# Performance work log

Measured on AMD Instinct MI355X. Metric: run time of the kernel, lower is better.

## Reference

```python
import jax, jax.numpy as jnp
import numpy as np

PAD = 0.1
RESO = 128           # plane_resolution
HID = 128            # hidden_dim
CDIM = 128           # c_dim
NBLK = 5             # n_blocks
PLANES = (('xz', (0, 2)), ('xy', (0, 1)), ('yz', (1, 2)))


def normalize_coordinate(p, dims):
    # p: (B,T,3) -> (B,T,2) in [0, 1)
    xy = p[..., list(dims)] / (1.0 + PAD + 1e-3) + 0.5
    return jnp.clip(xy, 0.0, 1.0 - 1e-5)


def coordinate2index(xy, reso):
    g = (xy * reso).astype(jnp.int32)          # (B,T,2)
    return g[..., 0] + reso * g[..., 1]        # (B,T) flat cell index


def scatter_max_gather(vals, idx, n_cells):
    # vals: (B,T,F), idx: (B,T) -> per-cell max gathered back to points (B,T,F)
    B, T, F = vals.shape
    flat_idx = (idx + jnp.arange(B, dtype=idx.dtype)[:, None] * n_cells).reshape(-1)
    fea = jax.ops.segment_max(vals.reshape(B * T, F), flat_idx, num_segments=B * n_cells)
    return fea[flat_idx].reshape(B, T, F)


def scatter_mean_plane(c, idx, n_cells):
    # c: (B,T,C), idx: (B,T) -> (B, n_cells, C); empty cells stay 0
    B, T, C = c.shape
    flat_idx = (idx + jnp.arange(B, dtype=idx.dtype)[:, None] * n_cells).reshape(-1)
    s = jax.ops.segment_sum(c.reshape(B * T, C), flat_idx, num_segments=B * n_cells)
    cnt = jax.ops.segment_sum(jnp.ones((B * T,), c.dtype), flat_idx, num_segments=B * n_cells)
    return (s / jnp.maximum(cnt, 1.0)[:, None]).reshape(B, n_cells, C)


def resnet_block(x, W0, b0, W1, b1, Ws):
    # ResnetBlockFC(2H -> H), size_h = H, shortcut = Linear(no bias)
    net = jax.nn.relu(x) @ W0 + b0
    dx = jax.nn.relu(net) @ W1 + b1
    return x @ Ws + dx


def setup_inputs() -> dict:
    key = jax.random.key(0)
    ks = jax.random.split(key, 10)
    B, T = 2, 32768
    s = 0.05
    return {
        'p': jax.random.uniform(ks[0], (B, T, 3), jnp.float32, -0.5, 0.5),
        'fc_pos_W': s * jax.random.normal(ks[1], (3, 2 * HID), jnp.float32),
        'fc_pos_b': s * jax.random.normal(ks[2], (2 * HID,), jnp.float32),
        'blocks_W0': s * jax.random.normal(ks[3], (NBLK, 2 * HID, HID), jnp.float32),
        'blocks_b0': s * jax.random.normal(ks[4], (NBLK, HID), jnp.float32),
        'blocks_W1': s * jax.random.normal(ks[5], (NBLK, HID, HID), jnp.float32),
        'blocks_b1': s * jax.random.normal(ks[6], (NBLK, HID), jnp.float32),
        'blocks_Ws': s * jax.random.normal(ks[7], (NBLK, 2 * HID, HID), jnp.float32),
        'fc_c_W': s * jax.random.normal(ks[8], (HID, CDIM), jnp.float32),
        'fc_c_b': s * jax.random.normal(ks[9], (CDIM,), jnp.float32),
    }


def reference(p, fc_pos_W, fc_pos_b, blocks_W0, blocks_b0, blocks_W1, blocks_b1,
              blocks_Ws, fc_c_W, fc_c_b):
    B, T, _ = p.shape
    R2 = RESO * RESO
    index = {k: coordinate2index(normalize_coordinate(p, d), RESO) for k, d in PLANES}

    net = p @ fc_pos_W + fc_pos_b                       # (B,T,2H)
    net = resnet_block(net, blocks_W0[0], blocks_b0[0],
                       blocks_W1[0], blocks_b1[0], blocks_Ws[0])  # (B,T,H)
    for i in range(1, NBLK):
        pooled = sum(scatter_max_gather(net, index[k], R2) for k, _ in PLANES)
        net = jnp.concatenate([net, pooled], axis=-1)   # (B,T,2H)
        net = resnet_block(net, blocks_W0[i], blocks_b0[i],
                           blocks_W1[i], blocks_b1[i], blocks_Ws[i])

    c = net @ fc_c_W + fc_c_b                           # (B,T,C)
    planes = []
    for k, _ in PLANES:  # order: xz, xy, yz
        fea = scatter_mean_plane(c, index[k], R2)       # (B,R2,C)
        planes.append(fea.transpose(0, 2, 1).reshape(B, CDIM, RESO, RESO))
    return jnp.stack(planes)                            # (3,B,C,R,R)
```

## Files before the change

kernel.cpp:

```cpp
#include <hip/hip_runtime.h>

#define TT 65536
#define R2 16384

typedef _Float16 f16x8 __attribute__((ext_vector_type(8)));
typedef float    f32x4 __attribute__((ext_vector_type(4)));
typedef unsigned u32x4 __attribute__((ext_vector_type(4)));

#define MFMA16 __builtin_amdgcn_mfma_f32_16x16x32_f16

__device__ __forceinline__ unsigned short f2h(float f){
    _Float16 h = (_Float16)f;
    return __builtin_bit_cast(unsigned short, h);
}
__device__ __forceinline__ float h2f(unsigned short u){
    return (float)__builtin_bit_cast(_Float16, u);
}
__device__ __forceinline__ unsigned relu2(unsigned w){
    unsigned s = w & 0x80008000u;
    unsigned mask = ((s >> 15) * 0x7FFFu) | s;
    return w & ~mask;
}
__device__ __forceinline__ float nrm(float a){
    float v = a / 1.101f + 0.5f;
    v = fmaxf(v, 0.0f);
    v = fminf(v, 0.99999f);
    return v;
}

__global__ __launch_bounds__(256) void k_repack(const float* __restrict__ W0,
        const float* __restrict__ W1, const float* __restrict__ Ws,
        const float* __restrict__ Wc, unsigned short* __restrict__ out,
        int* __restrict__ cnt){
    __shared__ unsigned short lh[4096];
    int b = blockIdx.x, tid = threadIdx.x;

    int gid = b*256 + tid;
    if (gid < 24576){ u32x4 z = {0,0,0,0}; ((u32x4*)cnt)[gid] = z; }

    const float* src; int obase;
    if (b < 100){
        int i = b/20, rr = b%20;
        if (rr < 8){       src = W0 + (size_t)i*32768 + rr*4096;      obase = i*81920 + rr*4096; }
        else if (rr < 12){ int ks=rr-8;  src = W1 + (size_t)i*16384 + ks*4096; obase = i*81920 + 32768 + ks*4096; }
        else {             int ks=rr-12; src = Ws + (size_t)i*32768 + ks*4096; obase = i*81920 + 49152 + ks*4096; }
    } else { int ks = b-100; src = Wc + ks*4096; obase = 409600 + ks*4096; }

    #pragma unroll
    for (int m = 0; m < 16; m++){
        int gi = m*256 + tid;
        lh[gi] = f2h(src[gi]);
    }
    __syncthreads();

    #pragma unroll
    for (int g2 = 0; g2 < 2; g2++){
        int base = tid*16 + g2*8;
        int l = (base >> 3) & 63, t = (base >> 9) & 7;
        int n = t*16 + (l & 15), kb = (l >> 4)*8;
        unsigned short h[8];
        #pragma unroll
        for (int j = 0; j < 8; j++) h[j] = lh[(kb + j)*128 + n];
        u32x4 pk;
        #pragma unroll
        for (int q = 0; q < 4; q++)
            pk[q] = (unsigned)h[2*q] | ((unsigned)h[2*q+1] << 16);
        *(u32x4*)(&out[obase + base]) = pk;
    }
}

__global__ __launch_bounds__(256) void k_idxhist(const float* __restrict__ p,
        int* __restrict__ idx, int* __restrict__ cnt){
    int pt = blockIdx.x*256 + threadIdx.x;
    float p0 = p[pt*3+0], p1 = p[pt*3+1], p2 = p[pt*3+2];
    int g0 = (int)(nrm(p0)*128.f);
    int g1 = (int)(nrm(p1)*128.f);
    int g2 = (int)(nrm(p2)*128.f);
    int i0 = g0 + 128*g2, i1 = g0 + 128*g1, i2 = g1 + 128*g2;
    idx[0*TT + pt] = i0;
    idx[1*TT + pt] = i1;
    idx[2*TT + pt] = i2;
    int b14 = (pt >> 15) << 14;
    atomicAdd(&cnt[0*32768 + b14 + i0], 1);
    atomicAdd(&cnt[1*32768 + b14 + i1], 1);
    atomicAdd(&cnt[2*32768 + b14 + i2], 1);
}

__global__ __launch_bounds__(1024) void k_scan(const int* __restrict__ cnt,
        int* __restrict__ cs, int* __restrict__ cp){
    __shared__ int wsum[16];
    int pl = blockIdx.x, tid = threadIdx.x;
    int lane = tid & 63, wid = tid >> 6;
    const int* c = cnt + pl*32768;
    int v[32], tot = 0;
    #pragma unroll
    for (int j = 0; j < 32; j++){ v[j] = c[tid*32 + j]; tot += v[j]; }
    int x = tot;
    #pragma unroll
    for (int off = 1; off < 64; off <<= 1){
        int y = __shfl_up(x, off, 64);
        if (lane >= off) x += y;
    }
    if (lane == 63) wsum[wid] = x;
    __syncthreads();
    int woff = 0;
    #pragma unroll
    for (int j = 0; j < 16; j++) woff += (j < wid) ? wsum[j] : 0;
    int run = woff + x - tot;
    #pragma unroll
    for (int j = 0; j < 32; j++){
        cs[pl*32769 + tid*32 + j] = run;
        cp[pl*32768 + tid*32 + j] = run;
        run += v[j];
    }
    if (tid == 1023) cs[pl*32769 + 32768] = TT;
}

__global__ __launch_bounds__(256) void k_scatter(const int* __restrict__ idx,
        int* __restrict__ cp, int* __restrict__ srt){
    int pt = blockIdx.x*256 + threadIdx.x;
    int b14 = (pt >> 15) << 14;
    #pragma unroll
    for (int pl = 0; pl < 3; pl++){
        int pos = atomicAdd(&cp[pl*32768 + b14 + idx[pl*TT + pt]], 1);
        srt[pl*TT + pos] = pt;
    }
}

__global__ __launch_bounds__(256) void k_pool3(const unsigned short* __restrict__ xb,
        const int* __restrict__ srt, const int* __restrict__ cs,
        unsigned short* __restrict__ mxp){
    int pl = blockIdx.y;
    const int* srtp = srt + (size_t)pl*TT;
    const int* csp  = cs  + (size_t)pl*32769;
    int lane = threadIdx.x & 63, w = threadIdx.x >> 6;
    int g = lane >> 4, l16 = lane & 15;
    int cbase = (blockIdx.x*4 + w)*4;
    for (int c = cbase; c < cbase + 4; c++){
        int s = csp[c], e = csp[c+1];
        if (s == e) continue;
        float fm[8];
        #pragma unroll
        for (int j = 0; j < 8; j++) fm[j] = -1e30f;
        for (int i = s + g; i < e; i += 4){
            int pt = srtp[i];
            u32x4 v = *(const u32x4*)(xb + (size_t)pt*256 + l16*8);
            #pragma unroll
            for (int q = 0; q < 4; q++){
                unsigned u = v[q];
                fm[2*q]   = fmaxf(fm[2*q],   h2f((unsigned short)(u & 0xFFFF)));
                fm[2*q+1] = fmaxf(fm[2*q+1], h2f((unsigned short)(u >> 16)));
            }
        }
        #pragma unroll
        for (int j = 0; j < 8; j++){
            fm[j] = fmaxf(fm[j], __shfl_xor(fm[j], 16, 64));
            fm[j] = fmaxf(fm[j], __shfl_xor(fm[j], 32, 64));
        }
        if (g == 0){
            u32x4 pk;
            #pragma unroll
            for (int q = 0; q < 4; q++)
                pk[q] = (unsigned)f2h(fm[2*q]) | ((unsigned)f2h(fm[2*q+1]) << 16);
            ((u32x4*)(mxp + ((size_t)pl*32768 + c)*128))[l16] = pk;
        }
    }
}

__global__ __launch_bounds__(256, 2) void k_resnet(unsigned short* __restrict__ xb,
        const unsigned short* __restrict__ wp,
        const float* __restrict__ b0, const float* __restrict__ b1,
        const int* __restrict__ idx, const unsigned short* __restrict__ mxp,
        const float* __restrict__ pin, const float* __restrict__ fW,
        const float* __restrict__ fb,
        const unsigned short* __restrict__ wc, const float* __restrict__ bc){
    __shared__ __align__(16) unsigned short lds[32768];
    unsigned short* lw = lds;
    unsigned short* lt = lds + 16384;
    int tid = threadIdx.x, w = tid >> 6, lane = tid & 63;
    int quad = lane >> 4, l15 = lane & 15;
    int m0 = blockIdx.x*128 + w*32;
    float b0v[8], b1v[8];
    #pragma unroll
    for (int t = 0; t < 8; t++){ b0v[t] = b0[t*16 + l15]; b1v[t] = b1[t*16 + l15]; }

    u32x4 pre[8];
    auto preload = [&](const unsigned short* src){
        const u32x4* g = (const u32x4*)src;
        #pragma unroll
        for (int i = 0; i < 8; i++) pre[i] = g[i*256 + tid];
    };
    auto flush = [&](){
        u32x4* l = (u32x4*)lw;
        #pragma unroll
        for (int i = 0; i < 8; i++) l[i*256 + tid] = pre[i];
    };

    preload(wp);

    u32x4 xf[2][4]; f16x8 pf[2][4];
    if (pin){
        #pragma unroll
        for (int s = 0; s < 2; s++){
            int row = m0 + s*16 + l15;
            float p0 = pin[row*3+0], p1 = pin[row*3+1], p2 = pin[row*3+2];
            #pragma unroll
            for (int ks = 0; ks < 4; ks++){
                int c0 = ks*32 + quad*8;
                unsigned short hx[8], hp[8];
                #pragma unroll
                for (int h = 0; h < 2; h++){
                    f32x4 w0 = *(const f32x4*)(fW + c0 + h*4);
                    f32x4 w1 = *(const f32x4*)(fW + 256 + c0 + h*4);
                    f32x4 w2 = *(const f32x4*)(fW + 512 + c0 + h*4);
                    f32x4 bb = *(const f32x4*)(fb + c0 + h*4);
                    f32x4 v0 = *(const f32x4*)(fW + 128 + c0 + h*4);
                    f32x4 v1 = *(const f32x4*)(fW + 384 + c0 + h*4);
                    f32x4 v2 = *(const f32x4*)(fW + 640 + c0 + h*4);
                    f32x4 bp = *(const f32x4*)(fb + 128 + c0 + h*4);
                    #pragma unroll
                    for (int j = 0; j < 4; j++){
                        hx[h*4+j] = f2h(bb[j] + p0*w0[j] + p1*w1[j] + p2*w2[j]);
                        hp[h*4+j] = f2h(bp[j] + p0*v0[j] + p1*v1[j] + p2*v2[j]);
                    }
                }
                unsigned short* dx = (unsigned short*)&xf[s][ks];
                unsigned short* dp = (unsigned short*)&pf[s][ks];
                #pragma unroll
                for (int j = 0; j < 8; j++){ dx[j] = hx[j]; dp[j] = hp[j]; }
            }
        }
    } else {
        #pragma unroll
        for (int s = 0; s < 2; s++){
            size_t rb = (size_t)(m0 + s*16 + l15)*256;
            #pragma unroll
            for (int ks = 0; ks < 4; ks++)
                xf[s][ks] = *(const u32x4*)(xb + rb + ks*32 + quad*8);
        }
        #pragma unroll
        for (int s = 0; s < 2; s++){
            int row = m0 + s*16 + l15;
            int b14 = (row >> 15) << 14;
            const unsigned short* q0 = mxp + ((size_t)(0*32768 + b14 + idx[row]))*128;
            const unsigned short* q1 = mxp + ((size_t)(1*32768 + b14 + idx[TT + row]))*128;
            const unsigned short* q2 = mxp + ((size_t)(2*32768 + b14 + idx[2*TT + row]))*128;
            #pragma unroll
            for (int ks = 0; ks < 4; ks++){
                int col = ks*32 + quad*8;
                f16x8 a = *(const f16x8*)(q0 + col);
                f16x8 b = *(const f16x8*)(q1 + col);
                f16x8 c = *(const f16x8*)(q2 + col);
                f16x8 r;
                #pragma unroll
                for (int j = 0; j < 8; j++)
                    r[j] = (_Float16)((float)a[j] + (float)b[j] + (float)c[j]);
                pf[s][ks] = r;
            }
        }
    }

    f32x4 acc[2][8];
    #pragma unroll
    for (int s = 0; s < 2; s++)
        #pragma unroll
        for (int t = 0; t < 8; t++){ f32x4 z = {0.f,0.f,0.f,0.f}; acc[s][t] = z; }

    __syncthreads(); flush(); __syncthreads();
    preload(wp + 16384);
    {
        #pragma unroll
        for (int ks = 0; ks < 4; ks++){
            u32x4 u0 = xf[0][ks], u1 = xf[1][ks];
            u0.x = relu2(u0.x); u0.y = relu2(u0.y); u0.z = relu2(u0.z); u0.w = relu2(u0.w);
            u1.x = relu2(u1.x); u1.y = relu2(u1.y); u1.z = relu2(u1.z); u1.w = relu2(u1.w);
            f16x8 a0 = __builtin_bit_cast(f16x8, u0);
            f16x8 a1 = __builtin_bit_cast(f16x8, u1);
            #pragma unroll
            for (int t = 0; t < 8; t++){
                f16x8 b = *(const f16x8*)&lw[((ks*8 + t)*64 + lane)*8];
                acc[0][t] = MFMA16(a0, b, acc[0][t], 0, 0, 0);
                acc[1][t] = MFMA16(a1, b, acc[1][t], 0, 0, 0);
            }
        }
    }

    __syncthreads(); flush(); __syncthreads();
    preload(wp + 32768);
    {
        #pragma unroll
        for (int ks = 0; ks < 4; ks++){
            u32x4 u0 = __builtin_bit_cast(u32x4, pf[0][ks]);
            u32x4 u1 = __builtin_bit_cast(u32x4, pf[1][ks]);
            u0.x = relu2(u0.x); u0.y = relu2(u0.y); u0.z = relu2(u0.z); u0.w = relu2(u0.w);
            u1.x = relu2(u1.x); u1.y = relu2(u1.y); u1.z = relu2(u1.z); u1.w = relu2(u1.w);
            f16x8 a0 = __builtin_bit_cast(f16x8, u0);
            f16x8 a1 = __builtin_bit_cast(f16x8, u1);
            #pragma unroll
            for (int t = 0; t < 8; t++){
                f16x8 b = *(const f16x8*)&lw[((ks*8 + t)*64 + lane)*8];
                acc[0][t] = MFMA16(a0, b, acc[0][t], 0, 0, 0);
                acc[1][t] = MFMA16(a1, b, acc[1][t], 0, 0, 0);
            }
        }
    }

    __syncthreads(); flush(); __syncthreads();
    preload(wp + 49152);
    f32x4 acc2[2][8];
    #pragma unroll
    for (int s = 0; s < 2; s++){
        int strip = w*2 + s;
        #pragma unroll
        for (int t = 0; t < 8; t++){
            int ks2 = t >> 1;
            int l2b = ((t & 1)*2 + ((lane >> 3) & 1))*16 + quad*4;
            #pragma unroll
            for (int r = 0; r < 4; r++){
                float v = acc[s][t][r] + b0v[t];
                v = fmaxf(v, 0.f);
                lt[(((ks2*8 + strip)*64) + l2b + r)*8 + (lane & 7)] = f2h(v);
            }
        }
    }
    #pragma unroll
    for (int s = 0; s < 2; s++)
        #pragma unroll
        for (int t = 0; t < 8; t++){ f32x4 iv = {b1v[t],b1v[t],b1v[t],b1v[t]}; acc2[s][t] = iv; }
    #pragma unroll
    for (int ks = 0; ks < 4; ks++){
        f16x8 a0 = *(const f16x8*)&lt[((ks*8 + w*2 + 0)*64 + lane)*8];
        f16x8 a1 = *(const f16x8*)&lt[((ks*8 + w*2 + 1)*64 + lane)*8];
        #pragma unroll
        for (int t = 0; t < 8; t++){
            f16x8 b = *(const f16x8*)&lw[((ks*8 + t)*64 + lane)*8];
            acc2[0][t] = MFMA16(a0, b, acc2[0][t], 0, 0, 0);
            acc2[1][t] = MFMA16(a1, b, acc2[1][t], 0, 0, 0);
        }
    }

    __syncthreads(); flush(); __syncthreads();
    preload(wp + 65536);
    {
        #pragma unroll
        for (int ks = 0; ks < 4; ks++){
            f16x8 a0 = __builtin_bit_cast(f16x8, xf[0][ks]);
            f16x8 a1 = __builtin_bit_cast(f16x8, xf[1][ks]);
            #pragma unroll
            for (int t = 0; t < 8; t++){
                f16x8 b = *(const f16x8*)&lw[((ks*8 + t)*64 + lane)*8];
                acc2[0][t] = MFMA16(a0, b, acc2[0][t], 0, 0, 0);
                acc2[1][t] = MFMA16(a1, b, acc2[1][t], 0, 0, 0);
            }
        }
    }

    __syncthreads(); flush(); __syncthreads();
    if (wc) preload(wc);
    {
        #pragma unroll
        for (int ks = 0; ks < 4; ks++){
            f16x8 a0 = pf[0][ks];
            f16x8 a1 = pf[1][ks];
            #pragma unroll
            for (int t = 0; t < 8; t++){
                f16x8 b = *(const f16x8*)&lw[((ks*8 + t)*64 + lane)*8];
                acc2[0][t] = MFMA16(a0, b, acc2[0][t], 0, 0, 0);
                acc2[1][t] = MFMA16(a1, b, acc2[1][t], 0, 0, 0);
            }
        }
    }

    if (!wc){
        #pragma unroll
        for (int s = 0; s < 2; s++)
            #pragma unroll
            for (int t = 0; t < 8; t++)
                #pragma unroll
                for (int r = 0; r < 4; r++){
                    int row = m0 + s*16 + quad*4 + r;
                    xb[(size_t)row*256 + t*16 + l15] = f2h(acc2[s][t][r]);
                }
        return;
    }

    __syncthreads(); flush(); __syncthreads();
    #pragma unroll
    for (int s = 0; s < 2; s++){
        int strip = w*2 + s;
        #pragma unroll
        for (int t = 0; t < 8; t++){
            int ks2 = t >> 1;
            int l2b = ((t & 1)*2 + ((lane >> 3) & 1))*16 + quad*4;
            #pragma unroll
            for (int r = 0; r < 4; r++)
                lt[(((ks2*8 + strip)*64) + l2b + r)*8 + (lane & 7)] = f2h(acc2[s][t][r]);
        }
    }
    f32x4 acc3[2][8];
    #pragma unroll
    for (int t = 0; t < 8; t++){
        float bv = bc[t*16 + l15];
        f32x4 iv = {bv, bv, bv, bv};
        acc3[0][t] = iv; acc3[1][t] = iv;
    }
    #pragma unroll
    for (int ks = 0; ks < 4; ks++){
        f16x8 a0 = *(const f16x8*)&lt[((ks*8 + w*2 + 0)*64 + lane)*8];
        f16x8 a1 = *(const f16x8*)&lt[((ks*8 + w*2 + 1)*64 + lane)*8];
        #pragma unroll
        for (int t = 0; t < 8; t++){
            f16x8 b = *(const f16x8*)&lw[((ks*8 + t)*64 + lane)*8];
            acc3[0][t] = MFMA16(a0, b, acc3[0][t], 0, 0, 0);
            acc3[1][t] = MFMA16(a1, b, acc3[1][t], 0, 0, 0);
        }
    }
    #pragma unroll
    for (int s = 0; s < 2; s++)
        #pragma unroll
        for (int t = 0; t < 8; t++)
            #pragma unroll
            for (int r = 0; r < 4; r++){
                int row = m0 + s*16 + quad*4 + r;
                xb[(size_t)row*256 + 128 + t*16 + l15] = f2h(acc3[s][t][r]);
            }
}

__global__ __launch_bounds__(256) void k_psum3(const unsigned short* __restrict__ xb,
        const int* __restrict__ srt, const int* __restrict__ cs,
        float* __restrict__ out){
    __shared__ float ls[32*129];
    int pl = blockIdx.y;
    const int* srtp = srt + (size_t)pl*TT;
    const int* csp  = cs  + (size_t)pl*32769;
    int tid = threadIdx.x;
    int lane = tid & 63, w = tid >> 6;
    int g = lane >> 4, l16 = lane & 15;
    int c0 = blockIdx.x * 32;
    for (int cc = w*8; cc < w*8 + 8; cc++){
        int c = c0 + cc;
        int s = csp[c], e = csp[c+1];
        float fs[8];
        #pragma unroll
        for (int j = 0; j < 8; j++) fs[j] = 0.f;
        for (int i = s + g; i < e; i += 4){
            int pt = srtp[i];
            u32x4 v = *(const u32x4*)(xb + (size_t)pt*256 + 128 + l16*8);
            #pragma unroll
            for (int q = 0; q < 4; q++){
                unsigned u = v[q];
                fs[2*q]   += h2f((unsigned short)(u & 0xFFFF));
                fs[2*q+1] += h2f((unsigned short)(u >> 16));
            }
        }
        #pragma unroll
        for (int j = 0; j < 8; j++){
            fs[j] += __shfl_xor(fs[j], 16, 64);
            fs[j] += __shfl_xor(fs[j], 32, 64);
        }
        float rc = (e > s) ? 1.f/(float)(e - s) : 0.f;
        if (g == 0){
            #pragma unroll
            for (int j = 0; j < 8; j++) ls[cc*129 + l16*8 + j] = fs[j]*rc;
        }
    }
    __syncthreads();
    int pb = pl*2 + (c0 >> 14);
    float* o = out + (size_t)pb*128*R2 + (c0 & 16383);
    #pragma unroll
    for (int k = 0; k < 16; k++){
        int lin = k*256 + tid;
        int f = lin >> 5, cc = lin & 31;
        o[(size_t)f*R2 + cc] = ls[cc*129 + f];
    }
}

extern "C" void kernel_launch(void* const* d_in, const int* in_sizes, int n_in,
                              void* d_out, int out_size, void* d_ws, size_t ws_size,
                              hipStream_t stream) {
    const float* p        = (const float*)d_in[0];
    const float* fc_pos_W = (const float*)d_in[1];
    const float* fc_pos_b = (const float*)d_in[2];
    const float* bW0      = (const float*)d_in[3];
    const float* bb0      = (const float*)d_in[4];
    const float* bW1      = (const float*)d_in[5];
    const float* bb1      = (const float*)d_in[6];
    const float* bWs      = (const float*)d_in[7];
    const float* fc_c_W   = (const float*)d_in[8];
    const float* fc_c_b   = (const float*)d_in[9];
    float* out = (float*)d_out;

    char* ws = (char*)d_ws;
    int*            idx   = (int*)ws;
    unsigned short* xbuf  = (unsigned short*)(ws + 786432);
    int*            srt   = (int*)(ws + 34340864);
    int*            cs    = (int*)(ws + 35127296);
    int*            cp    = (int*)(ws + 35520528);
    unsigned short* wpack = (unsigned short*)(ws + 35913744);
    unsigned short* mxp   = (unsigned short*)(ws + 36765712);

    k_repack <<<104, 256, 0, stream>>>(bW0, bW1, bWs, fc_c_W, wpack, cp);
    k_idxhist<<<TT/256, 256, 0, stream>>>(p, idx, cp);
    k_scan   <<<3, 1024, 0, stream>>>(cp, cs, cp);
    k_scatter<<<TT/256, 256, 0, stream>>>(idx, cp, srt);

    k_resnet<<<512, 256, 0, stream>>>(xbuf, wpack, bb0, bb1,
            idx, (const unsigned short*)nullptr,
            p, fc_pos_W, fc_pos_b,
            (const unsigned short*)nullptr, (const float*)nullptr);

    for (int i = 1; i < 5; i++){
        k_pool3<<<dim3(2048, 3), 256, 0, stream>>>(xbuf, srt, cs, mxp);
        const unsigned short* wc = (i == 4) ? (wpack + 409600) : (const unsigned short*)nullptr;
        const float* bcp = (i == 4) ? fc_c_b : (const float*)nullptr;
        k_resnet<<<512, 256, 0, stream>>>(xbuf, wpack + (size_t)i*81920,
                bb0 + (size_t)i*128, bb1 + (size_t)i*128,
                idx, mxp,
                (const float*)nullptr, (const float*)nullptr, (const float*)nullptr,
                wc, bcp);
    }

    k_psum3<<<dim3(1024, 3), 256, 0, stream>>>(xbuf, srt, cs, out);
}
```

Measured before the change: 376.6 us.

## Fuse per-cell max pooling into resnet kernel with ping-pong activation buffers

Removes the separate k_pool3 kernel and its mxp buffer. Each resnet block now computes the per-cell max for its own rows by walking the sorted point list of every plane and reading neighbor activations directly. Activations use ping-pong input/output buffers so the fused gather does not race with writes. This saves four launches and the pooled-buffer round trip, but cells are recomputed redundantly (once per point in the cell) with serial per-lane loops, which adds gather traffic and divergence inside the MFMA kernel.

Result: slower. 447.7 us (+18.9%).

```diff
diff --git a/kernel.cpp b/kernel.cpp
--- a/kernel.cpp
+++ b/kernel.cpp
@@ -86,8 +86,8 @@
     atomicAdd(&cnt[2*32768 + b14 + i2], 1);
 }
 
-__global__ __launch_bounds__(1024) void k_scan(const int* __restrict__ cnt,
-        int* __restrict__ cs, int* __restrict__ cp){
+__global__ __launch_bounds__(1024) void k_scan(const int* cnt,
+        int* __restrict__ cs, int* cp){
     __shared__ int wsum[16];
     int pl = blockIdx.x, tid = threadIdx.x;
     int lane = tid & 63, wid = tid >> 6;
@@ -127,50 +127,35 @@
     }
 }
 
-__global__ __launch_bounds__(256) void k_pool3(const unsigned short* __restrict__ xb,
-        const int* __restrict__ srt, const int* __restrict__ cs,
-        unsigned short* __restrict__ mxp){
-    int pl = blockIdx.y;
-    const int* srtp = srt + (size_t)pl*TT;
-    const int* csp  = cs  + (size_t)pl*32769;
-    int lane = threadIdx.x & 63, w = threadIdx.x >> 6;
-    int g = lane >> 4, l16 = lane & 15;
-    int cbase = (blockIdx.x*4 + w)*4;
-    for (int c = cbase; c < cbase + 4; c++){
-        int s = csp[c], e = csp[c+1];
-        if (s == e) continue;
-        float fm[8];
-        #pragma unroll
-        for (int j = 0; j < 8; j++) fm[j] = -1e30f;
-        for (int i = s + g; i < e; i += 4){
-            int pt = srtp[i];
-            u32x4 v = *(const u32x4*)(xb + (size_t)pt*256 + l16*8);
-            #pragma unroll
-            for (int q = 0; q < 4; q++){
-                unsigned u = v[q];
-                fm[2*q]   = fmaxf(fm[2*q],   h2f((unsigned short)(u & 0xFFFF)));
-                fm[2*q+1] = fmaxf(fm[2*q+1], h2f((unsigned short)(u >> 16)));
-            }
-        }
-        #pragma unroll
-        for (int j = 0; j < 8; j++){
-            fm[j] = fmaxf(fm[j], __shfl_xor(fm[j], 16, 64));
-            fm[j] = fmaxf(fm[j], __shfl_xor(fm[j], 32, 64));
-        }
-        if (g == 0){
-            u32x4 pk;
-            #pragma unroll
-            for (int q = 0; q < 4; q++)
-                pk[q] = (unsigned)f2h(fm[2*q]) | ((unsigned)f2h(fm[2*q+1]) << 16);
-            ((u32x4*)(mxp + ((size_t)pl*32768 + c)*128))[l16] = pk;
-        }
-    }
-}
-
-__global__ __launch_bounds__(256, 2) void k_resnet(unsigned short* __restrict__ xb,
+__device__ __forceinline__ void cellmax(const unsigned short* __restrict__ xin,
+        const int* __restrict__ srtp, int st, int en, int coff, f16x8 mp[4]){
+    #pragma unroll
+    for (int ks = 0; ks < 4; ks++){
+        f16x8 z;
+        #pragma unroll
+        for (int j = 0; j < 8; j++) z[j] = (_Float16)(-65504.f);
+        mp[ks] = z;
+    }
+    for (int i = st; i < en; i++){
+        int pt = srtp[i];
+        const unsigned short* q = xin + (size_t)pt*128 + coff;
+        #pragma unroll
+        for (int ks = 0; ks < 4; ks++){
+            f16x8 v = *(const f16x8*)(q + ks*32);
+            #pragma unroll
+            for (int j = 0; j < 8; j++)
+                mp[ks][j] = (v[j] > mp[ks][j]) ? v[j] : mp[ks][j];
+        }
+    }
+}
+
+__global__ __launch_bounds__(256, 2) void k_resnet(
+        const unsigned short* __restrict__ xin,
+        unsigned short* __restrict__ xout,
         const unsigned short* __restrict__ wp,
         const float* __restrict__ b0, const float* __restrict__ b1,
-        const int* __restrict__ idx, const unsigned short* __restrict__ mxp,
+        const int* __restrict__ idx, const int* __restrict__ srt,
+        const int* __restrict__ cs,
         const float* __restrict__ pin, const float* __restrict__ fW,
         const float* __restrict__ fb,
         const unsigned short* __restrict__ wc, const float* __restrict__ bc){
@@ -233,28 +218,29 @@
     } else {
         #pragma unroll
         for (int s = 0; s < 2; s++){
-            size_t rb = (size_t)(m0 + s*16 + l15)*256;
+            int row = m0 + s*16 + l15;
+            size_t rb = (size_t)row*128;
             #pragma unroll
             for (int ks = 0; ks < 4; ks++)
-                xf[s][ks] = *(const u32x4*)(xb + rb + ks*32 + quad*8);
+                xf[s][ks] = *(const u32x4*)(xin + rb + ks*32 + quad*8);
         }
         #pragma unroll
         for (int s = 0; s < 2; s++){
             int row = m0 + s*16 + l15;
             int b14 = (row >> 15) << 14;
-            const unsigned short* q0 = mxp + ((size_t)(0*32768 + b14 + idx[row]))*128;
-            const unsigned short* q1 = mxp + ((size_t)(1*32768 + b14 + idx[TT + row]))*128;
-            const unsigned short* q2 = mxp + ((size_t)(2*32768 + b14 + idx[2*TT + row]))*128;
+            int c0i = b14 + idx[0*TT + row];
+            int c1i = b14 + idx[1*TT + row];
+            int c2i = b14 + idx[2*TT + row];
+            f16x8 mp0[4], mp1[4], mp2[4];
+            cellmax(xin, srt + 0*TT, cs[0*32769 + c0i], cs[0*32769 + c0i + 1], quad*8, mp0);
+            cellmax(xin, srt + 1*TT, cs[1*32769 + c1i], cs[1*32769 + c1i + 1], quad*8, mp1);
+            cellmax(xin, srt + 2*TT, cs[2*32769 + c2i], cs[2*32769 + c2i + 1], quad*8, mp2);
             #pragma unroll
             for (int ks = 0; ks < 4; ks++){
-                int col = ks*32 + quad*8;
-                f16x8 a = *(const f16x8*)(q0 + col);
-                f16x8 b = *(const f16x8*)(q1 + col);
-                f16x8 c = *(const f16x8*)(q2 + col);
                 f16x8 r;
                 #pragma unroll
                 for (int j = 0; j < 8; j++)
-                    r[j] = (_Float16)((float)a[j] + (float)b[j] + (float)c[j]);
+                    r[j] = (_Float16)((float)mp0[ks][j] + (float)mp1[ks][j] + (float)mp2[ks][j]);
                 pf[s][ks] = r;
             }
         }
@@ -379,7 +365,7 @@
                 #pragma unroll
                 for (int r = 0; r < 4; r++){
                     int row = m0 + s*16 + quad*4 + r;
-                    xb[(size_t)row*256 + t*16 + l15] = f2h(acc2[s][t][r]);
+                    xout[(size_t)row*128 + t*16 + l15] = f2h(acc2[s][t][r]);
                 }
         return;
     }
@@ -422,11 +408,11 @@
             #pragma unroll
             for (int r = 0; r < 4; r++){
                 int row = m0 + s*16 + quad*4 + r;
-                xb[(size_t)row*256 + 128 + t*16 + l15] = f2h(acc3[s][t][r]);
-            }
-}
-
-__global__ __launch_bounds__(256) void k_psum3(const unsigned short* __restrict__ xb,
+                xout[(size_t)row*128 + t*16 + l15] = f2h(acc3[s][t][r]);
+            }
+}
+
+__global__ __launch_bounds__(256) void k_psum3(const unsigned short* __restrict__ cb,
         const int* __restrict__ srt, const int* __restrict__ cs,
         float* __restrict__ out){
     __shared__ float ls[32*129];
@@ -445,7 +431,7 @@
         for (int j = 0; j < 8; j++) fs[j] = 0.f;
         for (int i = s + g; i < e; i += 4){
             int pt = srtp[i];
-            u32x4 v = *(const u32x4*)(xb + (size_t)pt*256 + 128 + l16*8);
+            u32x4 v = *(const u32x4*)(cb + (size_t)pt*128 + l16*8);
             #pragma unroll
             for (int q = 0; q < 4; q++){
                 unsigned u = v[q];
@@ -492,33 +478,33 @@
 
     char* ws = (char*)d_ws;
     int*            idx   = (int*)ws;
-    unsigned short* xbuf  = (unsigned short*)(ws + 786432);
-    int*            srt   = (int*)(ws + 34340864);
-    int*            cs    = (int*)(ws + 35127296);
-    int*            cp    = (int*)(ws + 35520528);
-    unsigned short* wpack = (unsigned short*)(ws + 35913744);
-    unsigned short* mxp   = (unsigned short*)(ws + 36765712);
+    unsigned short* net0  = (unsigned short*)(ws + 786432);
+    unsigned short* net1  = (unsigned short*)(ws + 17563648);
+    unsigned short* cbuf  = (unsigned short*)(ws + 34340864);
+    int*            srt   = (int*)(ws + 51118080);
+    int*            cs    = (int*)(ws + 51904512);
+    int*            cp    = (int*)(ws + 52297744);
+    unsigned short* wpack = (unsigned short*)(ws + 52690960);
+
+    const unsigned short* NUS = (const unsigned short*)nullptr;
+    const float* NF = (const float*)nullptr;
 
     k_repack <<<104, 256, 0, stream>>>(bW0, bW1, bWs, fc_c_W, wpack, cp);
-    k_idxhist<<<TT/256, 256, 0, stream>>>(p, idx, cp);
+    k_idxhist<<<256, 256, 0, stream>>>(p, idx, cp);
     k_scan   <<<3, 1024, 0, stream>>>(cp, cs, cp);
-    k_scatter<<<TT/256, 256, 0, stream>>>(idx, cp, srt);
-
-    k_resnet<<<512, 256, 0, stream>>>(xbuf, wpack, bb0, bb1,
-            idx, (const unsigned short*)nullptr,
-            p, fc_pos_W, fc_pos_b,
-            (const unsigned short*)nullptr, (const float*)nullptr);
-
-    for (int i = 1; i < 5; i++){
-        k_pool3<<<dim3(2048, 3), 256, 0, stream>>>(xbuf, srt, cs, mxp);
-        const unsigned short* wc = (i == 4) ? (wpack + 409600) : (const unsigned short*)nullptr;
-        const float* bcp = (i == 4) ? fc_c_b : (const float*)nullptr;
-        k_resnet<<<512, 256, 0, stream>>>(xbuf, wpack + (size_t)i*81920,
-                bb0 + (size_t)i*128, bb1 + (size_t)i*128,
-                idx, mxp,
-                (const float*)nullptr, (const float*)nullptr, (const float*)nullptr,
-                wc, bcp);
-    }
-
-    k_psum3<<<dim3(1024, 3), 256, 0, stream>>>(xbuf, srt, cs, out);
-}
+    k_scatter<<<256, 256, 0, stream>>>(idx, cp, srt);
+
+    k_resnet<<<512, 256, 0, stream>>>(NUS, net0, wpack, bb0, bb1,
+            idx, srt, cs, p, fc_pos_W, fc_pos_b, NUS, NF);
+    k_resnet<<<512, 256, 0, stream>>>(net0, net1, wpack + 81920,
+            bb0 + 128, bb1 + 128, idx, srt, cs, NF, NF, NF, NUS, NF);
+    k_resnet<<<512, 256, 0, stream>>>(net1, net0, wpack + 163840,
+            bb0 + 256, bb1 + 256, idx, srt, cs, NF, NF, NF, NUS, NF);
+    k_resnet<<<512, 256, 0, stream>>>(net0, net1, wpack + 245760,
+            bb0 + 384, bb1 + 384, idx, srt, cs, NF, NF, NF, NUS, NF);
+    k_resnet<<<512, 256, 0, stream>>>(net1, cbuf, wpack + 327680,
+            bb0 + 512, bb1 + 512, idx, srt, cs, NF, NF, NF,
+            wpack + 409600, fc_c_b);
+
+    k_psum3<<<dim3(1024, 3), 256, 0, stream>>>(cbuf, srt, cs, out);
+}
```

## Double-buffer weight tiles in LDS and ping-pong compact net buffers

Applied to the files above, without the earlier changes.

The resnet kernel now keeps two LDS weight buffers, so the next weight slab is flushed while the current GEMM runs, halving the barriers per stage. The second GEMM's hidden activations are staged through a small per-k-slice LDS tile instead of a full 32 KB tile. The net activations move from one 256-wide interleaved buffer to ping-pong 128-wide buffers plus a separate c buffer, which makes rows dense for pool and psum gathers. LDS use grows to 72 KB per block, which may hurt occupancy at two blocks per CU, and the workspace footprint grows.

New measurement: 389.2 us. +3.3%, slower.

```diff
diff --git a/kernel.cpp b/kernel.cpp
--- a/kernel.cpp
+++ b/kernel.cpp
@@ -86,8 +86,8 @@
     atomicAdd(&cnt[2*32768 + b14 + i2], 1);
 }
 
-__global__ __launch_bounds__(1024) void k_scan(const int* __restrict__ cnt,
-        int* __restrict__ cs, int* __restrict__ cp){
+__global__ __launch_bounds__(1024) void k_scan(const int* cnt,
+        int* __restrict__ cs, int* cp){
     __shared__ int wsum[16];
     int pl = blockIdx.x, tid = threadIdx.x;
     int lane = tid & 63, wid = tid >> 6;
@@ -144,7 +144,7 @@
         for (int j = 0; j < 8; j++) fm[j] = -1e30f;
         for (int i = s + g; i < e; i += 4){
             int pt = srtp[i];
-            u32x4 v = *(const u32x4*)(xb + (size_t)pt*256 + l16*8);
+            u32x4 v = *(const u32x4*)(xb + (size_t)pt*128 + l16*8);
             #pragma unroll
             for (int q = 0; q < 4; q++){
                 unsigned u = v[q];
@@ -167,16 +167,19 @@
     }
 }
 
-__global__ __launch_bounds__(256, 2) void k_resnet(unsigned short* __restrict__ xb,
+__global__ __launch_bounds__(256, 2) void k_resnet(
+        const unsigned short* __restrict__ xin,
+        unsigned short* __restrict__ xout,
         const unsigned short* __restrict__ wp,
         const float* __restrict__ b0, const float* __restrict__ b1,
         const int* __restrict__ idx, const unsigned short* __restrict__ mxp,
         const float* __restrict__ pin, const float* __restrict__ fW,
         const float* __restrict__ fb,
         const unsigned short* __restrict__ wc, const float* __restrict__ bc){
-    __shared__ __align__(16) unsigned short lds[32768];
-    unsigned short* lw = lds;
-    unsigned short* lt = lds + 16384;
+    __shared__ __align__(16) unsigned short lds[36864];
+    unsigned short* lw0 = lds;
+    unsigned short* lw1 = lds + 16384;
+    unsigned short* lt  = lds + 32768;
     int tid = threadIdx.x, w = tid >> 6, lane = tid & 63;
     int quad = lane >> 4, l15 = lane & 15;
     int m0 = blockIdx.x*128 + w*32;
@@ -190,10 +193,22 @@
         #pragma unroll
         for (int i = 0; i < 8; i++) pre[i] = g[i*256 + tid];
     };
-    auto flush = [&](){
-        u32x4* l = (u32x4*)lw;
+    auto flushto = [&](unsigned short* dst){
+        u32x4* l = (u32x4*)dst;
         #pragma unroll
         for (int i = 0; i < 8; i++) l[i*256 + tid] = pre[i];
+    };
+    auto gemm = [&](const f16x8* a0, const f16x8* a1, const unsigned short* lwx,
+                    f32x4 (&ac)[2][8]){
+        #pragma unroll
+        for (int ks = 0; ks < 4; ks++){
+            #pragma unroll
+            for (int t = 0; t < 8; t++){
+                f16x8 b = *(const f16x8*)&lwx[((ks*8 + t)*64 + lane)*8];
+                ac[0][t] = MFMA16(a0[ks], b, ac[0][t], 0, 0, 0);
+                ac[1][t] = MFMA16(a1[ks], b, ac[1][t], 0, 0, 0);
+            }
+        }
     };
 
     preload(wp);
@@ -233,10 +248,10 @@
     } else {
         #pragma unroll
         for (int s = 0; s < 2; s++){
-            size_t rb = (size_t)(m0 + s*16 + l15)*256;
+            size_t rb = (size_t)(m0 + s*16 + l15)*128;
             #pragma unroll
             for (int ks = 0; ks < 4; ks++)
-                xf[s][ks] = *(const u32x4*)(xb + rb + ks*32 + quad*8);
+                xf[s][ks] = *(const u32x4*)(xin + rb + ks*32 + quad*8);
         }
         #pragma unroll
         for (int s = 0; s < 2; s++){
@@ -260,116 +275,89 @@
         }
     }
 
+    f16x8 rx[2][4], rp[2][4];
+    #pragma unroll
+    for (int s = 0; s < 2; s++)
+        #pragma unroll
+        for (int ks = 0; ks < 4; ks++){
+            u32x4 u = xf[s][ks];
+            u.x = relu2(u.x); u.y = relu2(u.y); u.z = relu2(u.z); u.w = relu2(u.w);
+            rx[s][ks] = __builtin_bit_cast(f16x8, u);
+            u32x4 v = __builtin_bit_cast(u32x4, pf[s][ks]);
+            v.x = relu2(v.x); v.y = relu2(v.y); v.z = relu2(v.z); v.w = relu2(v.w);
+            rp[s][ks] = __builtin_bit_cast(f16x8, v);
+        }
+
     f32x4 acc[2][8];
     #pragma unroll
     for (int s = 0; s < 2; s++)
         #pragma unroll
         for (int t = 0; t < 8; t++){ f32x4 z = {0.f,0.f,0.f,0.f}; acc[s][t] = z; }
 
-    __syncthreads(); flush(); __syncthreads();
+    flushto(lw0);
     preload(wp + 16384);
-    {
-        #pragma unroll
-        for (int ks = 0; ks < 4; ks++){
-            u32x4 u0 = xf[0][ks], u1 = xf[1][ks];
-            u0.x = relu2(u0.x); u0.y = relu2(u0.y); u0.z = relu2(u0.z); u0.w = relu2(u0.w);
-            u1.x = relu2(u1.x); u1.y = relu2(u1.y); u1.z = relu2(u1.z); u1.w = relu2(u1.w);
-            f16x8 a0 = __builtin_bit_cast(f16x8, u0);
-            f16x8 a1 = __builtin_bit_cast(f16x8, u1);
-            #pragma unroll
-            for (int t = 0; t < 8; t++){
-                f16x8 b = *(const f16x8*)&lw[((ks*8 + t)*64 + lane)*8];
-                acc[0][t] = MFMA16(a0, b, acc[0][t], 0, 0, 0);
-                acc[1][t] = MFMA16(a1, b, acc[1][t], 0, 0, 0);
-            }
-        }
-    }
-
-    __syncthreads(); flush(); __syncthreads();
+    __syncthreads();
+
+    flushto(lw1);
     preload(wp + 32768);
-    {
-        #pragma unroll
-        for (int ks = 0; ks < 4; ks++){
-            u32x4 u0 = __builtin_bit_cast(u32x4, pf[0][ks]);
-            u32x4 u1 = __builtin_bit_cast(u32x4, pf[1][ks]);
-            u0.x = relu2(u0.x); u0.y = relu2(u0.y); u0.z = relu2(u0.z); u0.w = relu2(u0.w);
-            u1.x = relu2(u1.x); u1.y = relu2(u1.y); u1.z = relu2(u1.z); u1.w = relu2(u1.w);
-            f16x8 a0 = __builtin_bit_cast(f16x8, u0);
-            f16x8 a1 = __builtin_bit_cast(f16x8, u1);
-            #pragma unroll
-            for (int t = 0; t < 8; t++){
-                f16x8 b = *(const f16x8*)&lw[((ks*8 + t)*64 + lane)*8];
-                acc[0][t] = MFMA16(a0, b, acc[0][t], 0, 0, 0);
-                acc[1][t] = MFMA16(a1, b, acc[1][t], 0, 0, 0);
-            }
-        }
-    }
-
-    __syncthreads(); flush(); __syncthreads();
+    gemm(rx[0], rx[1], lw0, acc);
+    __syncthreads();
+
+    flushto(lw0);
     preload(wp + 49152);
+    gemm(rp[0], rp[1], lw1, acc);
+    __syncthreads();
+
+    flushto(lw1);
+    preload(wp + 65536);
     f32x4 acc2[2][8];
     #pragma unroll
-    for (int s = 0; s < 2; s++){
-        int strip = w*2 + s;
+    for (int s = 0; s < 2; s++)
+        #pragma unroll
+        for (int t = 0; t < 8; t++){ f32x4 iv = {b1v[t],b1v[t],b1v[t],b1v[t]}; acc2[s][t] = iv; }
+    #pragma unroll
+    for (int k2 = 0; k2 < 4; k2++){
+        if (k2) asm volatile("s_waitcnt lgkmcnt(0)" ::: "memory");
+        #pragma unroll
+        for (int s = 0; s < 2; s++){
+            int strip = w*2 + s;
+            #pragma unroll
+            for (int tt = 0; tt < 2; tt++){
+                int t = k2*2 + tt;
+                int l2b = (tt*2 + ((lane >> 3) & 1))*16 + quad*4;
+                #pragma unroll
+                for (int r = 0; r < 4; r++){
+                    float v = fmaxf(acc[s][t][r] + b0v[t], 0.f);
+                    lt[((strip*64) + l2b + r)*8 + (lane & 7)] = f2h(v);
+                }
+            }
+        }
+        f16x8 a0 = *(const f16x8*)&lt[((w*2 + 0)*64 + lane)*8];
+        f16x8 a1 = *(const f16x8*)&lt[((w*2 + 1)*64 + lane)*8];
         #pragma unroll
         for (int t = 0; t < 8; t++){
-            int ks2 = t >> 1;
-            int l2b = ((t & 1)*2 + ((lane >> 3) & 1))*16 + quad*4;
-            #pragma unroll
-            for (int r = 0; r < 4; r++){
-                float v = acc[s][t][r] + b0v[t];
-                v = fmaxf(v, 0.f);
-                lt[(((ks2*8 + strip)*64) + l2b + r)*8 + (lane & 7)] = f2h(v);
-            }
-        }
-    }
-    #pragma unroll
-    for (int s = 0; s < 2; s++)
-        #pragma unroll
-        for (int t = 0; t < 8; t++){ f32x4 iv = {b1v[t],b1v[t],b1v[t],b1v[t]}; acc2[s][t] = iv; }
-    #pragma unroll
-    for (int ks = 0; ks < 4; ks++){
-        f16x8 a0 = *(const f16x8*)&lt[((ks*8 + w*2 + 0)*64 + lane)*8];
-        f16x8 a1 = *(const f16x8*)&lt[((ks*8 + w*2 + 1)*64 + lane)*8];
-        #pragma unroll
-        for (int t = 0; t < 8; t++){
-            f16x8 b = *(const f16x8*)&lw[((ks*8 + t)*64 + lane)*8];
+            f16x8 b = *(const f16x8*)&lw0[((k2*8 + t)*64 + lane)*8];
             acc2[0][t] = MFMA16(a0, b, acc2[0][t], 0, 0, 0);
             acc2[1][t] = MFMA16(a1, b, acc2[1][t], 0, 0, 0);
         }
     }
-
-    __syncthreads(); flush(); __syncthreads();
-    preload(wp + 65536);
-    {
-        #pragma unroll
-        for (int ks = 0; ks < 4; ks++){
-            f16x8 a0 = __builtin_bit_cast(f16x8, xf[0][ks]);
-            f16x8 a1 = __builtin_bit_cast(f16x8, xf[1][ks]);
-            #pragma unroll
-            for (int t = 0; t < 8; t++){
-                f16x8 b = *(const f16x8*)&lw[((ks*8 + t)*64 + lane)*8];
-                acc2[0][t] = MFMA16(a0, b, acc2[0][t], 0, 0, 0);
-                acc2[1][t] = MFMA16(a1, b, acc2[1][t], 0, 0, 0);
-            }
-        }
-    }
-
-    __syncthreads(); flush(); __syncthreads();
+    __syncthreads();
+
+    flushto(lw0);
     if (wc) preload(wc);
     {
+        f16x8 a0[4], a1[4];
         #pragma unroll
         for (int ks = 0; ks < 4; ks++){
-            f16x8 a0 = pf[0][ks];
-            f16x8 a1 = pf[1][ks];
-            #pragma unroll
-            for (int t = 0; t < 8; t++){
-                f16x8 b = *(const f16x8*)&lw[((ks*8 + t)*64 + lane)*8];
-                acc2[0][t] = MFMA16(a0, b, acc2[0][t], 0, 0, 0);
-                acc2[1][t] = MFMA16(a1, b, acc2[1][t], 0, 0, 0);
-            }
-        }
-    }
+            a0[ks] = __builtin_bit_cast(f16x8, xf[0][ks]);
+            a1[ks] = __builtin_bit_cast(f16x8, xf[1][ks]);
+        }
+        gemm(a0, a1, lw1, acc2);
+    }
+    __syncthreads();
+
+    if (wc) flushto(lw1);
+    gemm(pf[0], pf[1], lw0, acc2);
 
     if (!wc){
         #pragma unroll
@@ -379,24 +367,12 @@
                 #pragma unroll
                 for (int r = 0; r < 4; r++){
                     int row = m0 + s*16 + quad*4 + r;
-                    xb[(size_t)row*256 + t*16 + l15] = f2h(acc2[s][t][r]);
+                    xout[(size_t)row*128 + t*16 + l15] = f2h(acc2[s][t][r]);
                 }
         return;
     }
-
-    __syncthreads(); flush(); __syncthreads();
-    #pragma unroll
-    for (int s = 0; s < 2; s++){
-        int strip = w*2 + s;
-        #pragma unroll
-        for (int t = 0; t < 8; t++){
-            int ks2 = t >> 1;
-            int l2b = ((t & 1)*2 + ((lane >> 3) & 1))*16 + quad*4;
-            #pragma unroll
-            for (int r = 0; r < 4; r++)
-                lt[(((ks2*8 + strip)*64) + l2b + r)*8 + (lane & 7)] = f2h(acc2[s][t][r]);
-        }
-    }
+    __syncthreads();
+
     f32x4 acc3[2][8];
     #pragma unroll
     for (int t = 0; t < 8; t++){
@@ -405,12 +381,25 @@
         acc3[0][t] = iv; acc3[1][t] = iv;
     }
     #pragma unroll
-    for (int ks = 0; ks < 4; ks++){
-        f16x8 a0 = *(const f16x8*)&lt[((ks*8 + w*2 + 0)*64 + lane)*8];
-        f16x8 a1 = *(const f16x8*)&lt[((ks*8 + w*2 + 1)*64 + lane)*8];
+    for (int k2 = 0; k2 < 4; k2++){
+        asm volatile("s_waitcnt lgkmcnt(0)" ::: "memory");
+        #pragma unroll
+        for (int s = 0; s < 2; s++){
+            int strip = w*2 + s;
+            #pragma unroll
+            for (int tt = 0; tt < 2; tt++){
+                int t = k2*2 + tt;
+                int l2b = (tt*2 + ((lane >> 3) & 1))*16 + quad*4;
+                #pragma unroll
+                for (int r = 0; r < 4; r++)
+                    lt[((strip*64) + l2b + r)*8 + (lane & 7)] = f2h(acc2[s][t][r]);
+            }
+        }
+        f16x8 a0 = *(const f16x8*)&lt[((w*2 + 0)*64 + lane)*8];
+        f16x8 a1 = *(const f16x8*)&lt[((w*2 + 1)*64 + lane)*8];
         #pragma unroll
         for (int t = 0; t < 8; t++){
-            f16x8 b = *(const f16x8*)&lw[((ks*8 + t)*64 + lane)*8];
+            f16x8 b = *(const f16x8*)&lw1[((k2*8 + t)*64 + lane)*8];
             acc3[0][t] = MFMA16(a0, b, acc3[0][t], 0, 0, 0);
             acc3[1][t] = MFMA16(a1, b, acc3[1][t], 0, 0, 0);
         }
@@ -422,11 +411,11 @@
             #pragma unroll
             for (int r = 0; r < 4; r++){
                 int row = m0 + s*16 + quad*4 + r;
-                xb[(size_t)row*256 + 128 + t*16 + l15] = f2h(acc3[s][t][r]);
-            }
-}
-
-__global__ __launch_bounds__(256) void k_psum3(const unsigned short* __restrict__ xb,
+                xout[(size_t)row*128 + t*16 + l15] = f2h(acc3[s][t][r]);
+            }
+}
+
+__global__ __launch_bounds__(256) void k_psum3(const unsigned short* __restrict__ cb,
         const int* __restrict__ srt, const int* __restrict__ cs,
         float* __restrict__ out){
     __shared__ float ls[32*129];
@@ -445,7 +434,7 @@
         for (int j = 0; j < 8; j++) fs[j] = 0.f;
         for (int i = s + g; i < e; i += 4){
             int pt = srtp[i];
-            u32x4 v = *(const u32x4*)(xb + (size_t)pt*256 + 128 + l16*8);
+            u32x4 v = *(const u32x4*)(cb + (size_t)pt*128 + l16*8);
             #pragma unroll
             for (int q = 0; q < 4; q++){
                 unsigned u = v[q];
@@ -492,33 +481,39 @@
 
     char* ws = (char*)d_ws;
     int*            idx   = (int*)ws;
-    unsigned short* xbuf  = (unsigned short*)(ws + 786432);
-    int*            srt   = (int*)(ws + 34340864);
-    int*            cs    = (int*)(ws + 35127296);
-    int*            cp    = (int*)(ws + 35520528);
-    unsigned short* wpack = (unsigned short*)(ws + 35913744);
-    unsigned short* mxp   = (unsigned short*)(ws + 36765712);
+    unsigned short* net0  = (unsigned short*)(ws + 786432);
+    unsigned short* net1  = (unsigned short*)(ws + 17563648);
+    unsigned short* cbuf  = (unsigned short*)(ws + 34340864);
+    int*            srt   = (int*)(ws + 51118080);
+    int*            cs    = (int*)(ws + 51904512);
+    int*            cp    = (int*)(ws + 52297744);
+    unsigned short* wpack = (unsigned short*)(ws + 52690960);
+    unsigned short* mxp   = (unsigned short*)(ws + 53542928);
+
+    const unsigned short* NUS = (const unsigned short*)nullptr;
+    const float* NF = (const float*)nullptr;
 
     k_repack <<<104, 256, 0, stream>>>(bW0, bW1, bWs, fc_c_W, wpack, cp);
-    k_idxhist<<<TT/256, 256, 0, stream>>>(p, idx, cp);
+    k_idxhist<<<256, 256, 0, stream>>>(p, idx, cp);
     k_scan   <<<3, 1024, 0, stream>>>(cp, cs, cp);
-    k_scatter<<<TT/256, 256, 0, stream>>>(idx, cp, srt);
-
-    k_resnet<<<512, 256, 0, stream>>>(xbuf, wpack, bb0, bb1,
-            idx, (const unsigned short*)nullptr,
-            p, fc_pos_W, fc_pos_b,
-            (const unsigned short*)nullptr, (const float*)nullptr);
-
-    for (int i = 1; i < 5; i++){
-        k_pool3<<<dim3(2048, 3), 256, 0, stream>>>(xbuf, srt, cs, mxp);
-        const unsigned short* wc = (i == 4) ? (wpack + 409600) : (const unsigned short*)nullptr;
-        const float* bcp = (i == 4) ? fc_c_b : (const float*)nullptr;
-        k_resnet<<<512, 256, 0, stream>>>(xbuf, wpack + (size_t)i*81920,
-                bb0 + (size_t)i*128, bb1 + (size_t)i*128,
-                idx, mxp,
-                (const float*)nullptr, (const float*)nullptr, (const float*)nullptr,
-                wc, bcp);
-    }
-
-    k_psum3<<<dim3(1024, 3), 256, 0, stream>>>(xbuf, srt, cs, out);
-}
+    k_scatter<<<256, 256, 0, stream>>>(idx, cp, srt);
+
+    k_resnet<<<512, 256, 0, stream>>>(NUS, net0, wpack, bb0, bb1,
+            idx, NUS, p, fc_pos_W, fc_pos_b, NUS, NF);
+
+    k_pool3<<<dim3(2048, 3), 256, 0, stream>>>(net0, srt, cs, mxp);
+    k_resnet<<<512, 256, 0, stream>>>(net0, net1, wpack + 81920,
+            bb0 + 128, bb1 + 128, idx, mxp, NF, NF, NF, NUS, NF);
+    k_pool3<<<dim3(2048, 3), 256, 0, stream>>>(net1, srt, cs, mxp);
+    k_resnet<<<512, 256, 0, stream>>>(net1, net0, wpack + 163840,
+            bb0 + 256, bb1 + 256, idx, mxp, NF, NF, NF, NUS, NF);
+    k_pool3<<<dim3(2048, 3), 256, 0, stream>>>(net0, srt, cs, mxp);
+    k_resnet<<<512, 256, 0, stream>>>(net0, net1, wpack + 245760,
+            bb0 + 384, bb1 + 384, idx, mxp, NF, NF, NF, NUS, NF);
+    k_pool3<<<dim3(2048, 3), 256, 0, stream>>>(net1, srt, cs, mxp);
+    k_resnet<<<512, 256, 0, stream>>>(net1, cbuf, wpack + 327680,
+            bb0 + 512, bb1 + 512, idx, mxp, NF, NF, NF,
+            wpack + 409600, fc_c_b);
+
+    k_psum3<<<dim3(1024, 3), 256, 0, stream>>>(cbuf, srt, cs, out);
+}
```
